# Optimization experiments

Hardware: AMD Instinct MI355X
Metric: run time of the kernel (lower is better)

Reference implementation:

```python
import jax, jax.numpy as jnp
import numpy as np

WIN = 4096   # win_size == nfft
HOP = 2048   # hop_size == win_size // 2 (COLA)


def _hann_periodic(n):
    # torch.hann_window default is periodic
    return (0.5 * (1.0 - jnp.cos(2.0 * jnp.pi * jnp.arange(n) / n))).astype(jnp.float32)


def _stft(x):
    # x: [B, L] real. Pad to multiple of HOP (as in get_stft_torch), then
    # frame with center=False, apply periodic Hann, one-sided rfft.
    L = x.shape[-1]
    pad = (-L) % HOP
    x = jnp.pad(x, ((0, 0), (0, pad)))
    Lp = L + pad
    T = 1 + (Lp - WIN) // HOP  # number of frames, static
    idx = jnp.arange(T)[:, None] * HOP + jnp.arange(WIN)[None, :]
    frames = x[:, idx] * _hann_periodic(WIN)
    S = jnp.fft.rfft(frames, axis=-1)
    return jnp.swapaxes(S, -1, -2)  # [B, F, T]


def _edr_db(S):
    # Energy decay relief: suffix sum of |S|^2 over time, in dB.
    # Replaces the original O(T^2) per-frame loop with a reverse cumsum.
    p = (S.real * S.real + S.imag * S.imag).astype(jnp.float32)  # [B, F, T]
    suffix = jnp.cumsum(p[..., ::-1], axis=-1)[..., ::-1]
    return 10.0 * jnp.log10(suffix)  # db(x, is_squared=True)


def setup_inputs() -> dict:
    key = jax.random.key(0)
    k1, k2 = jax.random.split(key)
    B, NFREQ = 32, 192000
    return {
        "target_response": jax.random.normal(k1, (B, NFREQ), dtype=jnp.float32),
        "achieved_response": jax.random.normal(k2, (B, NFREQ), dtype=jnp.float32),
    }


def reference(target_response, achieved_response):
    n = target_response.shape[-1]
    # torch.fft.irfft(x, n=x.shape[-1]) -> time-domain RIR of length n
    target_rir = jnp.fft.irfft(target_response, n=n).astype(jnp.float32)
    achieved_rir = jnp.fft.irfft(achieved_response, n=n).astype(jnp.float32)

    S_target = _stft(target_rir)   # [B, F, T] complex64
    S_ach = _stft(achieved_rir)

    target_edr = _edr_db(S_target)  # [B, F, T] float32
    ach_edr = _edr_db(S_ach)

    freq_loss = jnp.sum(jnp.abs(target_edr - ach_edr), axis=-1)  # [B, F]
    loss_per_item = jnp.sum(freq_loss, axis=-1) / jnp.sum(
        jnp.abs(target_edr), axis=(-2, -1)
    )  # [B]
    return jnp.sum(loss_per_item)
```

## Files before the change

kernel.cpp:

```cpp
#include <hip/hip_runtime.h>
#include <hip/hip_fp16.h>
#include <math.h>

#define NSIG 64
#define NROW 192000
#define NN   192000
#define LP   192512
#define NT   93
#define NF   2049
#define PT   (NT*NF)
#define NK2  188
#define TWO_PI 6.28318530717958647692f
#define SQ2H  0.70710678118654752440f

#define WS_P_OFF   0
#define WS_A_OFF   48782592ULL
#define WS_Y_OFF   73424128ULL
#define WS_ACC_OFF 98065664ULL

__device__ __forceinline__ float2 cmul(float2 a, float2 b) {
    return make_float2(a.x*b.x - a.y*b.y, a.x*b.y + a.y*b.x);
}
__device__ __forceinline__ float2 cadd(float2 a, float2 b) {
    return make_float2(a.x + b.x, a.y + b.y);
}
__device__ __forceinline__ float2 csub(float2 a, float2 b) {
    return make_float2(a.x - b.x, a.y - b.y);
}
__device__ __forceinline__ float2 mul_nI(float2 z) { return make_float2(z.y, -z.x); }
__device__ __forceinline__ float2 mul_pI(float2 z) { return make_float2(-z.y, z.x); }
__device__ __forceinline__ __half2 f2h(float2 v) { return __float22half2_rn(v); }
__device__ __forceinline__ float2 h2f(__half2 h) { return __half22float2(h); }

__device__ __forceinline__ void dft8(float2 (&x)[8]) {
    float2 e0 = cadd(x[0], x[4]), e1 = csub(x[0], x[4]);
    float2 e2 = cadd(x[2], x[6]), e3 = csub(x[2], x[6]);
    float2 E0 = cadd(e0, e2), E2 = csub(e0, e2);
    float2 E1 = cadd(e1, mul_nI(e3)), E3 = csub(e1, mul_nI(e3));
    float2 o0 = cadd(x[1], x[5]), o1 = csub(x[1], x[5]);
    float2 o2 = cadd(x[3], x[7]), o3 = csub(x[3], x[7]);
    float2 O0 = cadd(o0, o2), O2 = csub(o0, o2);
    float2 O1 = cadd(o1, mul_nI(o3)), O3 = csub(o1, mul_nI(o3));
    float2 W1 = make_float2(SQ2H*(O1.x + O1.y), SQ2H*(O1.y - O1.x));
    float2 W2 = mul_nI(O2);
    float2 W3 = make_float2(SQ2H*(O3.y - O3.x), -SQ2H*(O3.x + O3.y));
    x[0] = cadd(E0, O0); x[4] = csub(E0, O0);
    x[1] = cadd(E1, W1); x[5] = csub(E1, W1);
    x[2] = cadd(E2, W2); x[6] = csub(E2, W2);
    x[3] = cadd(E3, W3); x[7] = csub(E3, W3);
}

__device__ __forceinline__ void dft8i(float2 (&x)[8]) {
    float2 e0 = cadd(x[0], x[4]), e1 = csub(x[0], x[4]);
    float2 e2 = cadd(x[2], x[6]), e3 = csub(x[2], x[6]);
    float2 E0 = cadd(e0, e2), E2 = csub(e0, e2);
    float2 E1 = cadd(e1, mul_pI(e3)), E3 = csub(e1, mul_pI(e3));
    float2 o0 = cadd(x[1], x[5]), o1 = csub(x[1], x[5]);
    float2 o2 = cadd(x[3], x[7]), o3 = csub(x[3], x[7]);
    float2 O0 = cadd(o0, o2), O2 = csub(o0, o2);
    float2 O1 = cadd(o1, mul_pI(o3)), O3 = csub(o1, mul_pI(o3));
    float2 W1 = make_float2(SQ2H*(O1.x - O1.y), SQ2H*(O1.x + O1.y));
    float2 W2 = mul_pI(O2);
    float2 W3 = make_float2(-SQ2H*(O3.x + O3.y), SQ2H*(O3.x - O3.y));
    x[0] = cadd(E0, O0); x[4] = csub(E0, O0);
    x[1] = cadd(E1, W1); x[5] = csub(E1, W1);
    x[2] = cadd(E2, W2); x[6] = csub(E2, W2);
    x[3] = cadd(E3, W3); x[7] = csub(E3, W3);
}

#define S3C 0.86602540378443865f
__device__ __forceinline__ void dft3i(float2& x0, float2& x1, float2& x2) {
    float2 u = cadd(x1, x2), v = csub(x1, x2);
    float2 w = make_float2(x0.x - 0.5f*u.x, x0.y - 0.5f*u.y);
    x0 = cadd(x0, u);
    float2 iv = make_float2(-S3C * v.y, S3C * v.x);
    x1 = cadd(w, iv);
    x2 = csub(w, iv);
}

#define C51 0.30901699437494742f
#define S51 0.95105651629515357f
#define C52 (-0.80901699437494742f)
#define S52 0.58778525229247313f
__device__ __forceinline__ void dft5i(float2& x0, float2& x1, float2& x2,
                                      float2& x3, float2& x4) {
    float2 t1 = cadd(x1, x4), t2 = csub(x1, x4);
    float2 t3 = cadd(x2, x3), t4 = csub(x2, x3);
    float2 s0 = x0;
    x0 = make_float2(s0.x + t1.x + t3.x, s0.y + t1.y + t3.y);
    float2 A1 = make_float2(s0.x + C51*t1.x + C52*t3.x, s0.y + C51*t1.y + C52*t3.y);
    float2 B1 = make_float2(S51*t2.x + S52*t4.x, S51*t2.y + S52*t4.y);
    float2 A2 = make_float2(s0.x + C52*t1.x + C51*t3.x, s0.y + C52*t1.y + C51*t3.y);
    float2 B2 = make_float2(S52*t2.x - S51*t4.x, S52*t2.y - S51*t4.y);
    x1 = make_float2(A1.x - B1.y, A1.y + B1.x);
    x4 = make_float2(A1.x + B1.y, A1.y - B1.x);
    x2 = make_float2(A2.x - B2.y, A2.y + B2.x);
    x3 = make_float2(A2.x + B2.y, A2.y - B2.x);
}

#define SSTR 520
__global__ void __launch_bounds__(256) k_stage1(const float* __restrict__ X0,
                                                const float* __restrict__ X1,
                                                __half2* __restrict__ A) {
    const int kb   = blockIdx.x;
    const int sig  = blockIdx.y;
    const int base = kb * 16;
    const float* X = (sig < 32) ? (X0 + (size_t)sig * NROW)
                                : (X1 + (size_t)(sig - 32) * NROW);
    __shared__ float SR[8 * SSTR], SI[8 * SSTR];
    const int tid = threadIdx.x;
    const int row = tid & 7;
    const int ln  = tid >> 3;

    const int k2e0 = base + 2 * row;
    const int k2e  = (k2e0 < NK2) ? k2e0 : (NK2 - 1);
    const int k2o  = (k2e0 + 1 < NK2) ? (k2e0 + 1) : (NK2 - 1);

    #pragma unroll
    for (int m = 0; m < 16; ++m) {
        int i = ln + 32 * m;
        int ide = 375 * i + k2e;
        int ido = 375 * i + k2o;
        float xe = X[(ide <= 96000) ? ide : (NN - ide)];
        float xo = X[(ido <= 96000) ? ido : (NN - ido)];
        SR[SSTR * row + i] = xe;
        SI[SSTR * row + i] = xo;
    }
    __syncthreads();

    const int w = tid >> 6;
    const int l = tid & 63;
    float* sra = SR + SSTR * (2 * w);     float* sia = SI + SSTR * (2 * w);
    float* srb = SR + SSTR * (2 * w + 1); float* sib = SI + SSTR * (2 * w + 1);
    float2 xa[8], xb[8];

    #pragma unroll
    for (int n1 = 0; n1 < 8; ++n1) {
        int ad = l + 64 * n1;
        xa[n1] = make_float2(sra[ad], sia[ad]);
        xb[n1] = make_float2(srb[ad], sib[ad]);
    }
    dft8i(xa); dft8i(xb);
    {
        float sn, cs; __sincosf(TWO_PI * (float)l * (1.0f / 512.0f), &sn, &cs);
        float2 bw = make_float2(cs, sn), tw = bw;
        xa[1] = cmul(xa[1], tw); xb[1] = cmul(xb[1], tw);
        #pragma unroll
        for (int k = 2; k < 8; ++k) {
            tw = cmul(tw, bw);
            xa[k] = cmul(xa[k], tw); xb[k] = cmul(xb[k], tw);
        }
    }
    #pragma unroll
    for (int a2 = 0; a2 < 8; ++a2) {
        int ad = 64 * a2 + (l ^ (8 * a2));
        sra[ad] = xa[a2].x; sia[ad] = xa[a2].y;
        srb[ad] = xb[a2].x; sib[ad] = xb[a2].y;
    }
    __builtin_amdgcn_wave_barrier();

    const int l0 = l & 7, aa = l >> 3;
    #pragma unroll
    for (int l1 = 0; l1 < 8; ++l1) {
        int ad = 64 * aa + ((l0 + 8 * l1) ^ (8 * aa));
        xa[l1] = make_float2(sra[ad], sia[ad]);
        xb[l1] = make_float2(srb[ad], sib[ad]);
    }
    dft8i(xa); dft8i(xb);
    {
        float sn, cs; __sincosf(TWO_PI * (float)l0 * (1.0f / 64.0f), &sn, &cs);
        float2 bw = make_float2(cs, sn), tw = bw;
        xa[1] = cmul(xa[1], tw); xb[1] = cmul(xb[1], tw);
        #pragma unroll
        for (int k = 2; k < 8; ++k) {
            tw = cmul(tw, bw);
            xa[k] = cmul(xa[k], tw); xb[k] = cmul(xb[k], tw);
        }
    }
    #pragma unroll
    for (int b2 = 0; b2 < 8; ++b2) {
        int ad = 64 * b2 + 8 * aa + (l0 ^ b2);
        sra[ad] = xa[b2].x; sia[ad] = xa[b2].y;
        srb[ad] = xb[b2].x; sib[ad] = xb[b2].y;
    }
    __builtin_amdgcn_wave_barrier();

    const int a3 = l & 7, b3 = l >> 3;
    #pragma unroll
    for (int l0r = 0; l0r < 8; ++l0r) {
        int ad = 64 * b3 + 8 * a3 + (l0r ^ b3);
        xa[l0r] = make_float2(sra[ad], sia[ad]);
        xb[l0r] = make_float2(srb[ad], sib[ad]);
    }
    dft8i(xa); dft8i(xb);
    #pragma unroll
    for (int c = 0; c < 8; ++c) {
        int ad = a3 + 8 * b3 + 64 * c;
        sra[ad] = xa[c].x; sia[ad] = xa[c].y;
        srb[ad] = xb[c].x; sib[ad] = xb[c].y;
    }
    __syncthreads();

    if (k2e0 < NK2) {
        float sn, cs;
        __sincosf(TWO_PI * (float)(k2e * ln) * (1.0f / 192000.0f), &sn, &cs);
        float2 wke = make_float2(cs, sn);
        __sincosf(TWO_PI * (float)(32 * k2e) * (1.0f / 192000.0f), &sn, &cs);
        float2 ste = make_float2(cs, sn);
        __sincosf(TWO_PI * (float)(k2o * ln) * (1.0f / 192000.0f), &sn, &cs);
        float2 wko = make_float2(cs, sn);
        __sincosf(TWO_PI * (float)(32 * k2o) * (1.0f / 192000.0f), &sn, &cs);
        float2 sto = make_float2(cs, sn);
        const bool odd_ok = (k2e0 + 1 < NK2);
        __half2* Ae = A + ((size_t)sig * NK2 + k2e) * 512;
        __half2* Ao = A + ((size_t)sig * NK2 + k2o) * 512;
        const float* zr = SR + SSTR * row;
        const float* zi = SI + SSTR * row;
        #pragma unroll
        for (int m = 0; m < 16; ++m) {
            int k  = ln + 32 * m;
            int km = (512 - k) & 511;
            float2 Z  = make_float2(zr[k],  zi[k]);
            float2 Zm = make_float2(zr[km], zi[km]);
            float2 S = make_float2(Z.x + Zm.x, Z.y - Zm.y);
            float2 D = make_float2(Z.x - Zm.x, Z.y + Zm.y);
            float2 Xe = make_float2(0.5f * S.x, 0.5f * S.y);
            float2 Xo = make_float2(0.5f * D.y, -0.5f * D.x);
            Ae[k] = f2h(cmul(Xe, wke));
            if (odd_ok) Ao[k] = f2h(cmul(Xo, wko));
            wke = cmul(wke, ste);
            wko = cmul(wko, sto);
        }
    }
}

#define TT2 16
#define T1STR 17
__global__ void __launch_bounds__(256) k_stage2(const __half2* __restrict__ A,
                                                __half* __restrict__ Y) {
    const int t1b = blockIdx.x * TT2;
    const int sig = blockIdx.y;
    __shared__ float SRT[375 * T1STR], SIT[375 * T1STR];
    const int tid = threadIdx.x;

    if (blockIdx.x == 0) {
        for (int j = tid; j < 512; j += 256)
            Y[(size_t)sig * LP + NN + j] = __float2half(0.f);
    }

    for (int w = tid; w < 25 * TT2; w += 256) {
        int c = w >> 4, t1l = w & 15;
        float2 v[15];
        const __half2* As = A + (size_t)sig * (NK2 * 512) + t1b + t1l;
        #pragma unroll
        for (int a = 0; a < 15; ++a) {
            int k2 = 25 * a + c;
            if (k2 < NK2) {
                v[a] = h2f(As[(size_t)k2 * 512]);
            } else {
                float2 u = h2f(As[(size_t)(375 - k2) * 512]);
                v[a] = make_float2(u.x, -u.y);
            }
        }
        #pragma unroll
        for (int r = 0; r < 5; ++r) dft3i(v[r], v[r + 5], v[r + 10]);
        float2 tw[15];
        tw[0] = make_float2(1.f, 0.f);
        float sn, cs; __sincosf(TWO_PI * (float)c * (1.0f / 375.0f), &sn, &cs);
        float2 stp = make_float2(cs, sn);
        #pragma unroll
        for (int e = 1; e < 15; ++e) tw[e] = cmul(tw[e - 1], stp);
        #pragma unroll
        for (int e3 = 0; e3 < 3; ++e3) {
            float2 h0 = v[5 * e3], h1, h2, h3, h4;
            if (e3 == 0) { h1 = v[1]; h2 = v[2]; h3 = v[3]; h4 = v[4]; }
            else if (e3 == 1) {
                h1 = cmul(v[6],  make_float2(0.91354545764260090f, 0.40673664307580021f));
                h2 = cmul(v[7],  make_float2(0.66913060635885821f, 0.74314482547739424f));
                h3 = cmul(v[8],  make_float2(0.30901699437494742f, 0.95105651629515357f));
                h4 = cmul(v[9],  make_float2(-0.10452846326765347f, 0.99452189536827334f));
            } else {
                h1 = cmul(v[11], make_float2(0.66913060635885821f, 0.74314482547739424f));
                h2 = cmul(v[12], make_float2(-0.10452846326765347f, 0.99452189536827334f));
                h3 = cmul(v[13], make_float2(-0.80901699437494742f, 0.58778525229247313f));
                h4 = cmul(v[14], make_float2(-0.97814760073380564f, -0.20791169081775934f));
            }
            dft5i(h0, h1, h2, h3, h4);
            float2 o0 = cmul(h0, tw[e3]);
            float2 o1 = cmul(h1, tw[e3 + 3]);
            float2 o2 = cmul(h2, tw[e3 + 6]);
            float2 o3 = cmul(h3, tw[e3 + 9]);
            float2 o4 = cmul(h4, tw[e3 + 12]);
            int r0 = ((e3     ) * 25 + c) * T1STR + t1l;
            int r1 = ((e3 + 3 ) * 25 + c) * T1STR + t1l;
            int r2 = ((e3 + 6 ) * 25 + c) * T1STR + t1l;
            int r3 = ((e3 + 9 ) * 25 + c) * T1STR + t1l;
            int r4 = ((e3 + 12) * 25 + c) * T1STR + t1l;
            SRT[r0] = o0.x; SIT[r0] = o0.y;
            SRT[r1] = o1.x; SIT[r1] = o1.y;
            SRT[r2] = o2.x; SIT[r2] = o2.y;
            SRT[r3] = o3.x; SIT[r3] = o3.y;
            SRT[r4] = o4.x; SIT[r4] = o4.y;
        }
    }
    __syncthreads();

    if (tid < 15 * TT2) {
        int e = tid >> 4, t1l = tid & 15;
        float2 t[25];
        #pragma unroll
        for (int c = 0; c < 25; ++c) {
            int rr = (e * 25 + c) * T1STR + t1l;
            t[c] = make_float2(SRT[rr], SIT[rr]);
        }
        #pragma unroll
        for (int c2 = 0; c2 < 5; ++c2)
            dft5i(t[c2], t[c2 + 5], t[c2 + 10], t[c2 + 15], t[c2 + 20]);
        t[6]  = cmul(t[6],  make_float2(0.96858316112863108f, 0.24868988716485479f));
        t[11] = cmul(t[11], make_float2(0.87630668004386358f, 0.48175367410171532f));
        t[16] = cmul(t[16], make_float2(0.72896862742141155f, 0.68454710592868873f));
        t[21] = cmul(t[21], make_float2(0.53582679497899666f, 0.84432792550201508f));
        t[7]  = cmul(t[7],  make_float2(0.87630668004386358f, 0.48175367410171532f));
        t[12] = cmul(t[12], make_float2(0.53582679497899666f, 0.84432792550201508f));
        t[17] = cmul(t[17], make_float2(0.06279051952931337f, 0.99802672842827156f));
        t[22] = cmul(t[22], make_float2(-0.42577929156507272f, 0.90482705246601958f));
        t[8]  = cmul(t[8],  make_float2(0.72896862742141155f, 0.68454710592868873f));
        t[13] = cmul(t[13], make_float2(0.06279051952931337f, 0.99802672842827156f));
        t[18] = cmul(t[18], make_float2(-0.63742398974868975f, 0.77051324277578925f));
        t[23] = cmul(t[23], make_float2(-0.99211470131447788f, 0.12533323356430426f));
        t[9]  = cmul(t[9],  make_float2(0.53582679497899666f, 0.84432792550201508f));
        t[14] = cmul(t[14], make_float2(-0.42577929156507272f, 0.90482705246601958f));
        t[19] = cmul(t[19], make_float2(-0.99211470131447788f, 0.12533323356430426f));
        t[24] = cmul(t[24], make_float2(-0.63742398974868997f, -0.77051324277578903f));
        #pragma unroll
        for (int u5 = 0; u5 < 5; ++u5)
            dft5i(t[5*u5], t[5*u5 + 1], t[5*u5 + 2], t[5*u5 + 3], t[5*u5 + 4]);
        __half* yb = Y + (size_t)sig * LP + t1b + t1l;
        #pragma unroll
        for (int u5 = 0; u5 < 5; ++u5)
            #pragma unroll
            for (int u5p = 0; u5p < 5; ++u5p) {
                int d = u5 + 5 * u5p;
                yb[(size_t)(512 * (15 * d + e))] =
                    __float2half_rn(t[5 * u5 + u5p].x * (1.0f / 192000.0f));
            }
    }
}

__global__ void __launch_bounds__(256) k_stft(const __half* __restrict__ Y,
                                              float* __restrict__ P,
                                              float* __restrict__ ACC) {
    const int fr  = blockIdx.x;
    const int sig = blockIdx.y;
    const int lt  = threadIdx.x;
    __shared__ float SR[2560], SI[2560];
    __shared__ float2 wt2[32];
    float2 x[8];
    float2 base2048;

    if (fr == 0 && sig == 0 && lt < 64) ACC[lt] = 0.f;

    {
        const __half2* yb = (const __half2*)(Y + (size_t)sig * LP + (size_t)fr * 2048);
        float sn, cs;
        __sincosf(TWO_PI * (float)lt * (1.0f / 2048.0f), &sn, &cs);
        base2048 = make_float2(cs, sn);
        float2 ce = base2048;
        const float2 d1 = make_float2(0.99999882345170188f,
                                      0.00153398018628477f);
        float2 co = cmul(ce, d1);
        const float2 r45 = make_float2(SQ2H, SQ2H);
        #pragma unroll
        for (int r = 0; r < 8; ++r) {
            float2 v = h2f(yb[lt + 256 * r]);
            float we = 0.5f - 0.5f * ce.x;
            float wo = 0.5f - 0.5f * co.x;
            x[r] = make_float2(v.x * we, v.y * wo);
            ce = cmul(ce, r45);
            co = cmul(co, r45);
        }
    }
    dft8(x);
    {
        float2 b = make_float2(base2048.x, -base2048.y), tw = b;
        x[1] = cmul(x[1], tw);
        #pragma unroll
        for (int k = 2; k < 8; ++k) { tw = cmul(tw, b); x[k] = cmul(x[k], tw); }
    }
    #pragma unroll
    for (int k = 0; k < 8; ++k) { SR[k * 256 + lt] = x[k].x; SI[k * 256 + lt] = x[k].y; }
    if (lt < 32) {
        float sn, cs; __sincosf(-TWO_PI * (float)lt * (1.0f / 256.0f), &sn, &cs);
        wt2[lt] = make_float2(cs, sn);
    }
    __syncthreads();

    {
        const int k2 = lt >> 5, m1 = lt & 31;
        #pragma unroll
        for (int r = 0; r < 8; ++r) {
            int idx = k2 * 256 + m1 + 32 * r;
            x[r] = make_float2(SR[idx], SI[idx]);
        }
        dft8(x);
        float2 b = wt2[m1], tw = b;
        x[1] = cmul(x[1], tw);
        #pragma unroll
        for (int k = 2; k < 8; ++k) { tw = cmul(tw, b); x[k] = cmul(x[k], tw); }
        __syncthreads();
        #pragma unroll
        for (int j = 0; j < 8; ++j) {
            int idx = k2 * 288 + j * 36 + m1;
            SR[idx] = x[j].x; SI[idx] = x[j].y;
        }
    }
    __syncthreads();

    {
        const int k2 = lt >> 5, j2 = (lt >> 2) & 7, p1 = lt & 3;
        #pragma unroll
        for (int r = 0; r < 8; ++r) {
            int idx = k2 * 288 + j2 * 36 + p1 + 4 * r;
            x[r] = make_float2(SR[idx], SI[idx]);
        }
        dft8(x);
        float2 b = (p1 == 0) ? make_float2(1.f, 0.f)
                 : (p1 == 1) ? make_float2(0.98078528040323044f, -0.19509032201612827f)
                 : (p1 == 2) ? make_float2(0.92387953251128676f, -0.38268343236508977f)
                 :             make_float2(0.83146961230254524f, -0.55557023301960222f);
        float2 tw = b;
        x[1] = cmul(x[1], tw);
        #pragma unroll
        for (int k = 2; k < 8; ++k) { tw = cmul(tw, b); x[k] = cmul(x[k], tw); }
        __syncthreads();
        #pragma unroll
        for (int q = 0; q < 8; ++q) {
            int idx = 5 * (q * 64 + k2 * 8 + j2) + p1;
            SR[idx] = x[q].x; SI[idx] = x[q].y;
        }
    }
    __syncthreads();

    {
        float2 za[4], zb[4];
        #pragma unroll
        for (int p = 0; p < 4; ++p) {
            int ia = 5 * lt + p;
            za[p] = make_float2(SR[ia], SI[ia]);
            zb[p] = make_float2(SR[ia + 1280], SI[ia + 1280]);
        }
        __syncthreads();
        const int q2a = lt >> 6, k2 = (lt >> 3) & 7, j2 = lt & 7;
        const int kbase = k2 + 8 * j2;
        {
            float2 s0 = cadd(za[0], za[2]), s1 = csub(za[0], za[2]);
            float2 s2 = cadd(za[1], za[3]), s3 = csub(za[1], za[3]);
            float2 X0 = cadd(s0, s2), X2 = csub(s0, s2);
            float2 X1 = cadd(s1, mul_nI(s3)), X3 = csub(s1, mul_nI(s3));
            int ka = kbase + 64 * q2a;
            SR[ka]        = X0.x; SI[ka]        = X0.y;
            SR[ka + 512]  = X1.x; SI[ka + 512]  = X1.y;
            SR[ka + 1024] = X2.x; SI[ka + 1024] = X2.y;
            SR[ka + 1536] = X3.x; SI[ka + 1536] = X3.y;
        }
        {
            float2 s0 = cadd(zb[0], zb[2]), s1 = csub(zb[0], zb[2]);
            float2 s2 = cadd(zb[1], zb[3]), s3 = csub(zb[1], zb[3]);
            float2 X0 = cadd(s0, s2), X2 = csub(s0, s2);
            float2 X1 = cadd(s1, mul_nI(s3)), X3 = csub(s1, mul_nI(s3));
            int kb = kbase + 64 * (q2a + 4);
            SR[kb]        = X0.x; SI[kb]        = X0.y;
            SR[kb + 512]  = X1.x; SI[kb + 512]  = X1.y;
            SR[kb + 1024] = X2.x; SI[kb + 1024] = X2.y;
            SR[kb + 1536] = X3.x; SI[kb + 1536] = X3.y;
        }
    }
    __syncthreads();

    {
        float* pb = P + (size_t)sig * PT + (size_t)fr * NF;
        float c2 = sqrtf(0.5f * (1.f + base2048.x));
        float s2 = sqrtf(0.5f * (1.f - base2048.x));
        float2 wk = make_float2(c2, -s2);
        const float2 stp = make_float2(0.92387953251128676f,
                                       -0.38268343236508977f);
        #pragma unroll
        for (int j = 0; j < 8; ++j) {
            int k  = lt + 256 * j;
            int kc = (2048 - k) & 2047;
            float zr = SR[k],  zi = SI[k];
            float cr = SR[kc], ci = SI[kc];
            float Ex = 0.5f * (zr + cr), Ey = 0.5f * (zi - ci);
            float Ox = 0.5f * (zi + ci), Oy = -0.5f * (zr - cr);
            float Xx = Ex + wk.x * Ox - wk.y * Oy;
            float Xy = Ey + wk.x * Oy + wk.y * Ox;
            pb[k] = Xx * Xx + Xy * Xy;
            wk = cmul(wk, stp);
        }
        if (lt == 0) { float d0 = SR[0] - SI[0]; pb[2048] = d0 * d0; }
    }
}

__global__ void __launch_bounds__(256) k_edr(const float* __restrict__ P,
                                             float* __restrict__ ACC) {
    const int b = blockIdx.y;
    const int f = blockIdx.x * 256 + threadIdx.x;
    const bool act = (f < NF);
    const float* Pt = P + (size_t)b * PT;
    const float* Pa = P + (size_t)(b + 32) * PT;
    float st = 0.f, sa = 0.f, num = 0.f, den = 0.f;
    if (act) {
        for (int t = NT - 1; t >= 0; --t) {
            st += Pt[(size_t)t * NF + f];
            sa += Pa[(size_t)t * NF + f];
            float et = 10.f * log10f(st);
            float ea = 10.f * log10f(sa);
            num += fabsf(et - ea);
            den += fabsf(et);
        }
    }
    for (int off = 32; off > 0; off >>= 1) {
        num += __shfl_down(num, off);
        den += __shfl_down(den, off);
    }
    __shared__ float sn_[4], sd_[4];
    int wave = threadIdx.x >> 6, lane = threadIdx.x & 63;
    if (lane == 0) { sn_[wave] = num; sd_[wave] = den; }
    __syncthreads();
    if (threadIdx.x == 0) {
        float n = sn_[0] + sn_[1] + sn_[2] + sn_[3];
        float d = sd_[0] + sd_[1] + sd_[2] + sd_[3];
        atomicAdd(&ACC[2 * b], n);
        atomicAdd(&ACC[2 * b + 1], d);
    }
}

__global__ void k_final(const float* __restrict__ ACC, float* __restrict__ out) {
    int tid = threadIdx.x;
    float r = 0.f;
    if (tid < 32) r = ACC[2 * tid] / ACC[2 * tid + 1];
    for (int off = 32; off > 0; off >>= 1) r += __shfl_down(r, off);
    if (tid == 0) out[0] = r;
}

extern "C" void kernel_launch(void* const* d_in, const int* in_sizes, int n_in,
                              void* d_out, int out_size, void* d_ws, size_t ws_size,
                              hipStream_t stream) {
    const float* X0 = (const float*)d_in[0];
    const float* X1 = (const float*)d_in[1];
    float* out = (float*)d_out;

    char* base = (char*)d_ws;
    float*   P  = (float*)(base + WS_P_OFF);
    __half2* A  = (__half2*)(base + WS_A_OFF);
    __half*  Y  = (__half*)(base + WS_Y_OFF);
    float*   ACC = (float*)(base + WS_ACC_OFF);

    k_stage1<<<dim3(12, 64),   dim3(256), 0, stream>>>(X0, X1, A);
    k_stage2<<<dim3(32, 64),   dim3(256), 0, stream>>>(A, Y);
    k_stft  <<<dim3(93, 64),   dim3(256), 0, stream>>>(Y, P, ACC);
    k_edr   <<<dim3(9, 32),    dim3(256), 0, stream>>>(P, ACC);
    k_final <<<1, 64, 0, stream>>>(ACC, out);
}
```

Before: 96.05 us.

## Store STFT magnitudes as fp16 with padded stride and remap block indices

The STFT kernel now writes the magnitude |X| as fp16, with a row stride padded to 2050, instead of fp32 power. This halves the intermediate buffer traffic between the STFT and EDR kernels. The EDR kernel reads half2 pairs, handles two frequency bins per thread, and squares the values back to power. Stage1 and STFT now use a flattened 1D grid with the signal index in the low bits, which changes block scheduling order. Storing magnitudes in fp16 loses precision in the power sums feeding log10, which risks accuracy.

```diff
diff --git a/kernel.cpp b/kernel.cpp
--- a/kernel.cpp
+++ b/kernel.cpp
@@ -8,15 +8,16 @@
 #define LP   192512
 #define NT   93
 #define NF   2049
-#define PT   (NT*NF)
+#define PSTR 2050
+#define PTS  (NT*PSTR)
 #define NK2  188
 #define TWO_PI 6.28318530717958647692f
 #define SQ2H  0.70710678118654752440f
 
 #define WS_P_OFF   0
-#define WS_A_OFF   48782592ULL
-#define WS_Y_OFF   73424128ULL
-#define WS_ACC_OFF 98065664ULL
+#define WS_A_OFF   24403200ULL
+#define WS_Y_OFF   49044736ULL
+#define WS_ACC_OFF 73686272ULL
 
 __device__ __forceinline__ float2 cmul(float2 a, float2 b) {
     return make_float2(a.x*b.x - a.y*b.y, a.x*b.y + a.y*b.x);
@@ -102,8 +103,9 @@
 __global__ void __launch_bounds__(256) k_stage1(const float* __restrict__ X0,
                                                 const float* __restrict__ X1,
                                                 __half2* __restrict__ A) {
-    const int kb   = blockIdx.x;
-    const int sig  = blockIdx.y;
+    const int bid  = blockIdx.x;
+    const int sig  = bid & 63;
+    const int kb   = bid >> 6;
     const int base = kb * 16;
     const float* X = (sig < 32) ? (X0 + (size_t)sig * NROW)
                                 : (X1 + (size_t)(sig - 32) * NROW);
@@ -348,17 +350,18 @@
 }
 
 __global__ void __launch_bounds__(256) k_stft(const __half* __restrict__ Y,
-                                              float* __restrict__ P,
+                                              __half* __restrict__ P,
                                               float* __restrict__ ACC) {
-    const int fr  = blockIdx.x;
-    const int sig = blockIdx.y;
+    const int bid = blockIdx.x;
+    const int sig = bid & 63;
+    const int fr  = bid >> 6;
     const int lt  = threadIdx.x;
     __shared__ float SR[2560], SI[2560];
     __shared__ float2 wt2[32];
     float2 x[8];
     float2 base2048;
 
-    if (fr == 0 && sig == 0 && lt < 64) ACC[lt] = 0.f;
+    if (bid == 0 && lt < 64) ACC[lt] = 0.f;
 
     {
         const __half2* yb = (const __half2*)(Y + (size_t)sig * LP + (size_t)fr * 2048);
@@ -478,7 +481,7 @@
     __syncthreads();
 
     {
-        float* pb = P + (size_t)sig * PT + (size_t)fr * NF;
+        __half* pb = P + (size_t)sig * PTS + (size_t)fr * PSTR;
         float c2 = sqrtf(0.5f * (1.f + base2048.x));
         float s2 = sqrtf(0.5f * (1.f - base2048.x));
         float2 wk = make_float2(c2, -s2);
@@ -494,29 +497,41 @@
             float Ox = 0.5f * (zi + ci), Oy = -0.5f * (zr - cr);
             float Xx = Ex + wk.x * Ox - wk.y * Oy;
             float Xy = Ey + wk.x * Oy + wk.y * Ox;
-            pb[k] = Xx * Xx + Xy * Xy;
+            pb[k] = __float2half_rn(sqrtf(Xx * Xx + Xy * Xy));
             wk = cmul(wk, stp);
         }
-        if (lt == 0) { float d0 = SR[0] - SI[0]; pb[2048] = d0 * d0; }
-    }
-}
-
-__global__ void __launch_bounds__(256) k_edr(const float* __restrict__ P,
+        if (lt == 0) { float d0 = SR[0] - SI[0]; pb[2048] = __float2half_rn(fabsf(d0)); }
+    }
+}
+
+__global__ void __launch_bounds__(256) k_edr(const __half* __restrict__ P,
                                              float* __restrict__ ACC) {
     const int b = blockIdx.y;
-    const int f = blockIdx.x * 256 + threadIdx.x;
-    const bool act = (f < NF);
-    const float* Pt = P + (size_t)b * PT;
-    const float* Pa = P + (size_t)(b + 32) * PT;
-    float st = 0.f, sa = 0.f, num = 0.f, den = 0.f;
-    if (act) {
+    const int p = blockIdx.x * 256 + threadIdx.x;
+    const bool act0 = (p <= 1024);
+    const bool act1 = (p < 1024);
+    const __half2* Pt2 = (const __half2*)(P + (size_t)b * PTS);
+    const __half2* Pa2 = (const __half2*)(P + (size_t)(b + 32) * PTS);
+    float st0 = 0.f, st1 = 0.f, sa0 = 0.f, sa1 = 0.f;
+    float num = 0.f, den = 0.f;
+    if (act0) {
         for (int t = NT - 1; t >= 0; --t) {
-            st += Pt[(size_t)t * NF + f];
-            sa += Pa[(size_t)t * NF + f];
-            float et = 10.f * log10f(st);
-            float ea = 10.f * log10f(sa);
-            num += fabsf(et - ea);
-            den += fabsf(et);
+            float2 vt = h2f(Pt2[(size_t)t * (PSTR / 2) + p]);
+            float2 va = h2f(Pa2[(size_t)t * (PSTR / 2) + p]);
+            st0 += vt.x * vt.x;
+            sa0 += va.x * va.x;
+            float et0 = 10.f * log10f(st0);
+            float ea0 = 10.f * log10f(sa0);
+            num += fabsf(et0 - ea0);
+            den += fabsf(et0);
+            if (act1) {
+                st1 += vt.y * vt.y;
+                sa1 += va.y * va.y;
+                float et1 = 10.f * log10f(st1);
+                float ea1 = 10.f * log10f(sa1);
+                num += fabsf(et1 - ea1);
+                den += fabsf(et1);
+            }
         }
     }
     for (int off = 32; off > 0; off >>= 1) {
@@ -551,14 +566,14 @@
     float* out = (float*)d_out;
 
     char* base = (char*)d_ws;
-    float*   P  = (float*)(base + WS_P_OFF);
+    __half*  P  = (__half*)(base + WS_P_OFF);
     __half2* A  = (__half2*)(base + WS_A_OFF);
     __half*  Y  = (__half*)(base + WS_Y_OFF);
     float*   ACC = (float*)(base + WS_ACC_OFF);
 
-    k_stage1<<<dim3(12, 64),   dim3(256), 0, stream>>>(X0, X1, A);
+    k_stage1<<<dim3(768),      dim3(256), 0, stream>>>(X0, X1, A);
     k_stage2<<<dim3(32, 64),   dim3(256), 0, stream>>>(A, Y);
-    k_stft  <<<dim3(93, 64),   dim3(256), 0, stream>>>(Y, P, ACC);
-    k_edr   <<<dim3(9, 32),    dim3(256), 0, stream>>>(P, ACC);
+    k_stft  <<<dim3(5952),     dim3(256), 0, stream>>>(Y, P, ACC);
+    k_edr   <<<dim3(5, 32),    dim3(256), 0, stream>>>(P, ACC);
     k_final <<<1, 64, 0, stream>>>(ACC, out);
 }
```

Measured after the change: 117.5 us. 1.22x slower.
